# Performance work log

Measured on AMD Instinct MI355X. Metric: run time of the kernel, lower is better.

The kernel has to match this reference:

```python
import jax, jax.numpy as jnp
import numpy as np

N, D, K = 65536, 256, 4096
EPS = 1e-5
DECAY = 0.99
BN_MOMENTUM = 0.1


def setup_inputs() -> dict:
    key = jax.random.key(0)
    k1, k2, k3, k4, k5, k6 = jax.random.split(key, 6)
    return {
        "x": jax.random.normal(k1, (N, D), dtype=jnp.float32),
        "embedding": jax.random.normal(k2, (K, D), dtype=jnp.float32),
        "ema_cluster_size": jnp.zeros((K,), dtype=jnp.float32),
        "ema_w": jax.random.normal(k3, (K, D), dtype=jnp.float32),
        "running_mean": jax.random.normal(k4, (D,), dtype=jnp.float32) * 0.1,
        "running_var": jax.random.uniform(k5, (D,), dtype=jnp.float32, minval=0.5, maxval=1.5),
    }


def reference(x, embedding, ema_cluster_size, ema_w, running_mean, running_var):
    n_batch = x.shape[0]
    num_embeddings = embedding.shape[0]

    # BatchNorm1d (training mode, affine=False): normalize with batch stats
    mean = jnp.mean(x, axis=0)                       # [D]
    var = jnp.mean((x - mean) ** 2, axis=0)          # biased var, [D]
    xn = (x - mean) / jnp.sqrt(var + EPS)            # [N, D]
    # running stat updates (torch uses unbiased var for running_var)
    new_running_mean = (1.0 - BN_MOMENTUM) * running_mean + BN_MOMENTUM * mean
    var_unbiased = var * (n_batch / (n_batch - 1.0))
    new_running_var = (1.0 - BN_MOMENTUM) * running_var + BN_MOMENTUM * var_unbiased

    # squared euclidean distances [N, K]
    distances = (jnp.sum(xn ** 2, axis=1, keepdims=True)
                 + jnp.sum(embedding ** 2, axis=1)
                 - 2.0 * xn @ embedding.T)
    idx = jnp.argmin(distances, axis=1)              # [N]

    # one-hot scatter stats via segment_sum (== encodings.T contractions)
    counts = jax.ops.segment_sum(jnp.ones((n_batch,), dtype=x.dtype), idx,
                                 num_segments=num_embeddings)   # [K]
    dw = jax.ops.segment_sum(xn, idx, num_segments=num_embeddings)  # [K, D]

    # EMA updates
    new_cs = ema_cluster_size * DECAY + (1.0 - DECAY) * counts
    n_total = jnp.sum(new_cs)
    new_cs = (new_cs + 1e-5) / (n_total + num_embeddings * 1e-5) * n_total
    new_ema_w = ema_w * DECAY + (1.0 - DECAY) * dw
    new_embedding = new_ema_w / new_cs[:, None]

    running_std = jnp.sqrt(new_running_var + EPS)
    embedding_output = new_embedding * running_std[None, :] + new_running_mean[None, :]

    return (idx[:, None], new_embedding, embedding_output, new_cs, new_ema_w,
            new_running_mean, new_running_var)
```

## Files before the change

kernel.cpp:

```cpp
#include <hip/hip_runtime.h>
#include <cfloat>
#include <cmath>

#define NROWS 65536
#define DDIM 256
#define KDIM 4096

typedef short bf16x8 __attribute__((ext_vector_type(8)));
typedef float f32x4 __attribute__((ext_vector_type(4)));

constexpr float EPSV = 1e-5f;
constexpr float DECAYV = 0.99f;
constexpr float MOMV = 0.1f;
constexpr float DELTA = 1.0f;
constexpr int CAP = 16;
constexpr int SEG = 128;

constexpr size_t WS_CNT     = 0;
constexpr size_t WS_NFLAG   = WS_CNT + NROWS;
constexpr size_t WS_HIST    = WS_NFLAG + 64;
constexpr size_t WS_ZEND    = WS_HIST + KDIM;
constexpr size_t WS_START   = WS_ZEND;
constexpr size_t WS_FILLPOS = WS_START + KDIM;
constexpr size_t WS_SEGSTART= WS_FILLPOS + KDIM;
constexpr size_t WS_NSEG    = WS_SEGSTART + KDIM + 64;
constexpr size_t WS_SEGLIST = WS_NSEG + 64;
constexpr size_t WS_PARTSUM = WS_SEGLIST + 4672;
constexpr size_t WS_PARTSQ  = WS_PARTSUM + 2048 * DDIM;
constexpr size_t WS_MIDSUM  = WS_PARTSQ + 2048 * DDIM;
constexpr size_t WS_MIDSQ   = WS_MIDSUM + 256 * DDIM;
constexpr size_t WS_MEAN    = WS_MIDSQ + 256 * DDIM;
constexpr size_t WS_RSTD    = WS_MEAN + DDIM;
constexpr size_t WS_NRMEAN  = WS_RSTD + DDIM;
constexpr size_t WS_NRVAR   = WS_NRMEAN + DDIM;
constexpr size_t WS_BVEC    = WS_NRVAR + DDIM;
constexpr size_t WS_NCSRAW  = WS_BVEC + KDIM;
constexpr size_t WS_NTOT    = WS_NCSRAW + KDIM;
constexpr size_t WS_ROWINFO = WS_NTOT + 64;
constexpr size_t WS_IDX     = WS_ROWINFO + 8 * (size_t)NROWS;
constexpr size_t WS_ROWTHR  = WS_IDX + NROWS;
constexpr size_t WS_FLAG    = WS_ROWTHR + NROWS;
constexpr size_t WS_ROWLIST = WS_FLAG + NROWS;
constexpr size_t WS_CAND    = WS_ROWLIST + NROWS;
constexpr size_t WS_DWPART  = WS_CAND;
constexpr size_t WS_EPROW   = WS_CAND + (size_t)NROWS * CAP;
constexpr size_t WS_EIMG    = WS_EPROW + (size_t)KDIM * DDIM;
constexpr size_t WS_XIMG    = WS_EIMG + 524288;

constexpr size_t O_IDX   = 0;
constexpr size_t O_EMB   = NROWS;
constexpr size_t O_EOUT  = O_EMB + (size_t)KDIM * DDIM;
constexpr size_t O_CS    = O_EOUT + (size_t)KDIM * DDIM;
constexpr size_t O_EMAW  = O_CS + KDIM;
constexpr size_t O_RMEAN = O_EMAW + (size_t)KDIM * DDIM;
constexpr size_t O_RVAR  = O_RMEAN + DDIM;

__device__ inline unsigned bfpack(float a, float b) {
    unsigned ua = __float_as_uint(a), ub = __float_as_uint(b);
    ua = (ua + 0x7FFFu + ((ua >> 16) & 1u)) >> 16;
    ub = (ub + 0x7FFFu + ((ub >> 16) & 1u)) & 0xFFFF0000u;
    return (ua & 0xFFFFu) | ub;
}

__device__ inline float unpackval(float p) {
    return __uint_as_float(__float_as_uint(p) & 0xFFFFF000u);
}

#define GLOAD_LDS16(g, l) __builtin_amdgcn_global_load_lds(                       \
        (const __attribute__((address_space(1))) void*)(g),                        \
        (__attribute__((address_space(3))) void*)(l), 16, 0, 0)

__global__ __launch_bounds__(128) void k_bnpack(const float* __restrict__ x,
                                                float* __restrict__ ws) {
    const int t = threadIdx.x;
    const int b = blockIdx.x;
    char* ximg = (char*)(ws + WS_XIMG);
    float s0 = 0.f, s1 = 0.f, q0 = 0.f, q1 = 0.f;
    const int r0 = b * 32;
#pragma unroll 4
    for (int i = 0; i < 32; ++i) {
        const int r = r0 + i;
        const float2 v = *(const float2*)(x + (size_t)r * DDIM + 2 * t);
        s0 += v.x; s1 += v.y; q0 += v.x * v.x; q1 += v.y * v.y;
        const int db = (4 * t + ((r & 15) << 5)) & 511;
        *(unsigned*)(ximg + (size_t)r * 512 + db) = bfpack(v.x, v.y);
    }
    *(float2*)(ws + WS_PARTSUM + (size_t)b * DDIM + 2 * t) = make_float2(s0, s1);
    *(float2*)(ws + WS_PARTSQ  + (size_t)b * DDIM + 2 * t) = make_float2(q0, q1);
}

__global__ __launch_bounds__(256) void k_bn_mid(float* __restrict__ ws) {
    const int d = threadIdx.x, j = blockIdx.x;
    float s = 0.f, q = 0.f;
#pragma unroll
    for (int i = 0; i < 8; ++i) {
        s += ws[WS_PARTSUM + (size_t)(j * 8 + i) * DDIM + d];
        q += ws[WS_PARTSQ  + (size_t)(j * 8 + i) * DDIM + d];
    }
    ws[WS_MIDSUM + (size_t)j * DDIM + d] = s;
    ws[WS_MIDSQ  + (size_t)j * DDIM + d] = q;
}

__global__ __launch_bounds__(256) void k_bn_final(const float* __restrict__ rmean_in,
                                                  const float* __restrict__ rvar_in,
                                                  float* __restrict__ ws,
                                                  float* __restrict__ out) {
    const int d = threadIdx.x;
    float s = 0.f, sq = 0.f;
    for (int b = 0; b < 256; ++b) {
        s  += ws[WS_MIDSUM + (size_t)b * DDIM + d];
        sq += ws[WS_MIDSQ  + (size_t)b * DDIM + d];
    }
    const float mean = s / (float)NROWS;
    float var = sq / (float)NROWS - mean * mean;
    var = fmaxf(var, 0.f);
    const float rstd = 1.0f / sqrtf(var + EPSV);
    const float nrm  = (1.0f - MOMV) * rmean_in[d] + MOMV * mean;
    const float varu = var * ((float)NROWS / (float)(NROWS - 1));
    const float nrv  = (1.0f - MOMV) * rvar_in[d] + MOMV * varu;
    ws[WS_MEAN + d] = mean;
    ws[WS_RSTD + d] = rstd;
    ws[WS_NRMEAN + d] = nrm;
    ws[WS_NRVAR + d] = nrv;
    out[O_RMEAN + d] = nrm;
    out[O_RVAR + d] = nrv;
}

__global__ __launch_bounds__(128) void k_eprime(const float* __restrict__ emb,
                                                float* __restrict__ ws) {
    __shared__ float red[128];
    const int k = blockIdx.x, t = threadIdx.x;
    const int d0 = 2 * t, d1 = 2 * t + 1;
    const float em0 = emb[(size_t)k * DDIM + d0], em1 = emb[(size_t)k * DDIM + d1];
    const float rs0 = ws[WS_RSTD + d0], rs1 = ws[WS_RSTD + d1];
    const float mn0 = ws[WS_MEAN + d0], mn1 = ws[WS_MEAN + d1];
    const float e0 = em0 * rs0, e1 = em1 * rs1;
    ws[WS_EPROW + (size_t)k * DDIM + d0] = e0;
    ws[WS_EPROW + (size_t)k * DDIM + d1] = e1;
    char* img = (char*)(ws + WS_EIMG);
    const int db = (4 * t + ((k & 15) << 5)) & 511;
    *(unsigned*)(img + (size_t)k * 512 + db) = bfpack(e0, e1);
    red[t] = em0 * em0 + 2.f * mn0 * e0 + em1 * em1 + 2.f * mn1 * e1;
    __syncthreads();
    for (int s = 64; s > 0; s >>= 1) { if (t < s) red[t] += red[t + s]; __syncthreads(); }
    if (t == 0) ws[WS_BVEC + k] = red[0];
}

__global__ __launch_bounds__(256, 4) void k_gemm_min(float* __restrict__ ws) {
    extern __shared__ char smem[];
    const int t = threadIdx.x, lane = t & 63, w = t >> 6;
    const int l4 = lane & 15, kg = lane >> 4;
    const int tile = blockIdx.x >> 2;
    const int cq   = blockIdx.x & 3;
    const int rowbase = tile * 128 + w * 32;
    const char* ximg = (const char*)(ws + WS_XIMG);
    const char* eimg = (const char*)(ws + WS_EIMG) + (size_t)cq * 524288;
    const float* bvec = ws + WS_BVEC;

    bf16x8 a[2][8];
#pragma unroll
    for (int m = 0; m < 2; ++m) {
        const char* rp = ximg + (size_t)(rowbase + m * 16 + l4) * 512;
#pragma unroll
        for (int ts = 0; ts < 8; ++ts) {
            const int byte = ((kg * 16 + ts * 64) + (l4 << 5)) & 511;
            a[m][ts] = *(const bf16x8*)(rp + byte);
        }
    }

    float b1f[2][4], b2f[2][4];
#pragma unroll
    for (int m = 0; m < 2; ++m)
#pragma unroll
        for (int r = 0; r < 4; ++r) { b1f[m][r] = FLT_MAX; b2f[m][r] = FLT_MAX; }

#pragma unroll
    for (int rr = 0; rr < 4; ++rr) {
        const int off = rr * 4096 + w * 1024;
        GLOAD_LDS16(eimg + off + lane * 16, smem + off);
    }
    __syncthreads();

    for (int ch = 0; ch < 32; ++ch) {
        const char* cur = smem + (ch & 1) * 16384;
        if (ch + 1 < 32) {
            const char* src = eimg + (size_t)(ch + 1) * 16384;
            char* nb = smem + ((ch + 1) & 1) * 16384;
#pragma unroll
            for (int rr = 0; rr < 4; ++rr) {
                const int off = rr * 4096 + w * 1024;
                GLOAD_LDS16(src + off + lane * 16, nb + off);
            }
        }

        f32x4 acc[2][2];
#pragma unroll
        for (int m = 0; m < 2; ++m)
#pragma unroll
            for (int n = 0; n < 2; ++n) acc[m][n] = 0.f;

#pragma unroll
        for (int ts = 0; ts < 8; ++ts) {
            const int rot = ((kg * 16 + ts * 64) + (l4 << 5)) & 511;
            bf16x8 bfr[2];
#pragma unroll
            for (int n = 0; n < 2; ++n)
                bfr[n] = *(const bf16x8*)(cur + (n * 16 + l4) * 512 + rot);
#pragma unroll
            for (int m = 0; m < 2; ++m)
#pragma unroll
                for (int n = 0; n < 2; ++n)
                    acc[m][n] = __builtin_amdgcn_mfma_f32_16x16x32_bf16(a[m][ts], bfr[n], acc[m][n], 0, 0, 0);
        }

#pragma unroll
        for (int n = 0; n < 2; ++n) {
            const unsigned col = (unsigned)(cq * 1024 + ch * 32 + n * 16 + l4);
            const float bc = bvec[col];
#pragma unroll
            for (int m = 0; m < 2; ++m)
#pragma unroll
                for (int r = 0; r < 4; ++r) {
                    const float s = fmaf(-2.f, acc[m][n][r], bc);
                    const float p = __uint_as_float(
                        (__float_as_uint(s) & 0xFFFFF000u) | col);
                    b2f[m][r] = __builtin_amdgcn_fmed3f(p, b1f[m][r], b2f[m][r]);
                    b1f[m][r] = fminf(p, b1f[m][r]);
                }
        }
        __syncthreads();
    }

    float2* rowinfo = (float2*)(ws + WS_ROWINFO);
#pragma unroll
    for (int m = 0; m < 2; ++m)
#pragma unroll
        for (int r = 0; r < 4; ++r) {
            float v1 = b1f[m][r], v2 = b2f[m][r];
#pragma unroll
            for (int st = 1; st < 16; st <<= 1) {
                const float o1 = __shfl_xor(v1, st);
                const float o2 = __shfl_xor(v2, st);
                const float mm = fminf(v2, o2);
                v2 = __builtin_amdgcn_fmed3f(v1, o1, mm);
                v1 = fminf(v1, o1);
            }
            if (l4 == 0) {
                const int row = rowbase + m * 16 + kg * 4 + r;
                rowinfo[(size_t)row * 4 + cq] = make_float2(v1, v2);
            }
        }
}

__global__ __launch_bounds__(256) void k_flag(float* __restrict__ ws,
                                              float* __restrict__ out) {
    const int r = blockIdx.x * 256 + threadIdx.x;
    const float2* rowinfo = (const float2*)(ws + WS_ROWINFO);
    float2 q = rowinfo[(size_t)r * 4];
    float v1 = q.x, v2 = q.y;
#pragma unroll
    for (int c = 1; c < 4; ++c) {
        q = rowinfo[(size_t)r * 4 + c];
        const float mm = fminf(v2, q.y);
        v2 = __builtin_amdgcn_fmed3f(v1, q.x, mm);
        v1 = fminf(v1, q.x);
    }
    const float v1v = unpackval(v1);
    const int   i1  = (int)(__float_as_uint(v1) & 0xFFFu);
    ws[WS_ROWTHR + r] = v1v + DELTA;
    if (unpackval(v2) - v1v <= DELTA) {
        const int pos = atomicAdd((int*)(ws + WS_NFLAG), 1);
        ((int*)(ws + WS_FLAG))[pos] = r;
    } else {
        out[O_IDX + r] = (float)i1;
        ((int*)(ws + WS_IDX))[r] = i1;
        atomicAdd((int*)(ws + WS_HIST) + i1, 1);
    }
}

__global__ __launch_bounds__(256) void k_cand(float* __restrict__ ws) {
    extern __shared__ char smem[];
    const int t = threadIdx.x, lane = t & 63, w = t >> 6;
    const int l4 = lane & 15, kg = lane >> 4;
    const char* ximg = (const char*)(ws + WS_XIMG);
    const char* eimg0 = (const char*)(ws + WS_EIMG);
    const float* bvec = ws + WS_BVEC;
    const int* flag = (const int*)(ws + WS_FLAG);
    int* cnt = (int*)(ws + WS_CNT);
    int* cand = (int*)(ws + WS_CAND);
    const int nflag = *(const int*)(ws + WS_NFLAG);
    if (nflag == 0) return;
    const int ntiles = (nflag + 127) >> 7;
    const int nitems = ntiles * 8;

    for (int item = blockIdx.x; item < nitems; item += gridDim.x) {
        const int tile = item >> 3, slice = item & 7;
        const int base = tile * 128 + w * 32;
        const char* eimg = eimg0 + (size_t)slice * 262144;
        bf16x8 a[2][8];
        int frow[2][4];
        float thr[2][4];
#pragma unroll
        for (int m = 0; m < 2; ++m) {
            const int ia = base + m * 16 + l4;
            const int rowa = flag[ia < nflag ? ia : (nflag - 1)];
            const char* rp = ximg + (size_t)rowa * 512;
#pragma unroll
            for (int ts = 0; ts < 8; ++ts) {
                const int byte = ((kg * 16 + ts * 64) + ((rowa & 15) << 5)) & 511;
                a[m][ts] = *(const bf16x8*)(rp + byte);
            }
#pragma unroll
            for (int r = 0; r < 4; ++r) {
                const int ie = base + m * 16 + kg * 4 + r;
                const bool val = ie < nflag;
                const int rowe = flag[val ? ie : (nflag - 1)];
                frow[m][r] = rowe;
                thr[m][r] = val ? ws[WS_ROWTHR + rowe] : -FLT_MAX;
            }
        }
#pragma unroll
        for (int rr = 0; rr < 4; ++rr) {
            const int off = rr * 4096 + w * 1024;
            GLOAD_LDS16(eimg + off + lane * 16, smem + off);
        }
        __syncthreads();

        for (int ch = 0; ch < 16; ++ch) {
            const char* cur = smem + (ch & 1) * 16384;
            if (ch + 1 < 16) {
                const char* src = eimg + (size_t)(ch + 1) * 16384;
                char* nb = smem + ((ch + 1) & 1) * 16384;
#pragma unroll
                for (int rr = 0; rr < 4; ++rr) {
                    const int off = rr * 4096 + w * 1024;
                    GLOAD_LDS16(src + off + lane * 16, nb + off);
                }
            }
            f32x4 acc[2][2];
#pragma unroll
            for (int m = 0; m < 2; ++m)
#pragma unroll
                for (int n = 0; n < 2; ++n) acc[m][n] = 0.f;
#pragma unroll
            for (int ts = 0; ts < 8; ++ts) {
                const int rot = ((kg * 16 + ts * 64) + (l4 << 5)) & 511;
                bf16x8 bfr[2];
#pragma unroll
                for (int n = 0; n < 2; ++n)
                    bfr[n] = *(const bf16x8*)(cur + (n * 16 + l4) * 512 + rot);
#pragma unroll
                for (int m = 0; m < 2; ++m)
#pragma unroll
                    for (int n = 0; n < 2; ++n)
                        acc[m][n] = __builtin_amdgcn_mfma_f32_16x16x32_bf16(a[m][ts], bfr[n], acc[m][n], 0, 0, 0);
            }
#pragma unroll
            for (int n = 0; n < 2; ++n) {
                const int col = slice * 512 + ch * 32 + n * 16 + l4;
                const float bc = bvec[col];
#pragma unroll
                for (int m = 0; m < 2; ++m)
#pragma unroll
                    for (int r = 0; r < 4; ++r) {
                        const float s = fmaf(-2.f, acc[m][n][r], bc);
                        if (s <= thr[m][r]) {
                            const int rr2 = frow[m][r];
                            const int pos = atomicAdd(&cnt[rr2], 1);
                            if (pos < CAP) cand[(size_t)rr2 * CAP + pos] = col;
                        }
                    }
            }
            __syncthreads();
        }
    }
}

__global__ __launch_bounds__(256) void k_resolve_f(const float* __restrict__ x,
                                                   float* __restrict__ ws,
                                                   float* __restrict__ out) {
    const int t = threadIdx.x, lane = t & 63;
    const int gw = (blockIdx.x * 256 + t) >> 6;
    const int nflag = *(const int*)(ws + WS_NFLAG);
    const int* flag = (const int*)(ws + WS_FLAG);
    const int* cnt = (const int*)(ws + WS_CNT);
    const int* cand = (const int*)(ws + WS_CAND);
    const float* eprow = ws + WS_EPROW;
    const float* bvec = ws + WS_BVEC;
    int* idx_int = (int*)(ws + WS_IDX);
    for (int i = gw; i < nflag; i += 1024) {
        const int row = flag[i];
        const float4 xr = ((const float4*)(x + (size_t)row * DDIM))[lane];
        const int n = cnt[row];
        float bestv = FLT_MAX;
        int bestk = KDIM;
        if (n >= 1 && n <= CAP) {
            for (int c = 0; c < n; ++c) {
                const int k = cand[(size_t)row * CAP + c];
                const float4 er = ((const float4*)(eprow + (size_t)k * DDIM))[lane];
                float p = xr.x * er.x + xr.y * er.y + xr.z * er.z + xr.w * er.w;
                p += __shfl_xor(p, 32); p += __shfl_xor(p, 16); p += __shfl_xor(p, 8);
                p += __shfl_xor(p, 4);  p += __shfl_xor(p, 2);  p += __shfl_xor(p, 1);
                const float s = fmaf(-2.f, p, bvec[k]);
                if (s < bestv || (s == bestv && k < bestk)) { bestv = s; bestk = k; }
            }
        } else {
            for (int k = 0; k < KDIM; ++k) {
                const float4 er = ((const float4*)(eprow + (size_t)k * DDIM))[lane];
                float p = xr.x * er.x + xr.y * er.y + xr.z * er.z + xr.w * er.w;
                p += __shfl_xor(p, 32); p += __shfl_xor(p, 16); p += __shfl_xor(p, 8);
                p += __shfl_xor(p, 4);  p += __shfl_xor(p, 2);  p += __shfl_xor(p, 1);
                const float s = fmaf(-2.f, p, bvec[k]);
                if (s < bestv || (s == bestv && k < bestk)) { bestv = s; bestk = k; }
            }
        }
        if (lane == 0) {
            out[O_IDX + row] = (float)bestk;
            idx_int[row] = bestk;
            atomicAdd((int*)(ws + WS_HIST) + bestk, 1);
        }
    }
}

__global__ __launch_bounds__(256) void k_scan(const float* __restrict__ cs_in,
                                              float* __restrict__ ws) {
    __shared__ int lsum[256], lseg[256];
    __shared__ float redf[256];
    const int t = threadIdx.x;
    const int* hist = (const int*)(ws + WS_HIST);
    int h[16];
    int s = 0, g = 0;
#pragma unroll
    for (int i = 0; i < 16; ++i) {
        h[i] = hist[t * 16 + i];
        s += h[i];
        g += (h[i] + SEG - 1) / SEG;
    }
    lsum[t] = s; lseg[t] = g;
    __syncthreads();
    int v = s, u = g;
    for (int off = 1; off < 256; off <<= 1) {
        const int av = (t >= off) ? lsum[t - off] : 0;
        const int au = (t >= off) ? lseg[t - off] : 0;
        __syncthreads();
        v += av; u += au;
        lsum[t] = v; lseg[t] = u;
        __syncthreads();
    }
    int runs = v - s, rung = u - g;
    int* start = (int*)(ws + WS_START);
    int* fillpos = (int*)(ws + WS_FILLPOS);
    int* segst = (int*)(ws + WS_SEGSTART);
    int* seglist = (int*)(ws + WS_SEGLIST);
    float emapart = 0.f;
#pragma unroll
    for (int i = 0; i < 16; ++i) {
        const int k = t * 16 + i;
        start[k] = runs;
        fillpos[k] = runs;
        segst[k] = rung;
        const int ns = (h[i] + SEG - 1) / SEG;
        for (int j = 0; j < ns; ++j) seglist[rung + j] = (k << 10) | j;
        runs += h[i];
        rung += ns;
        const float ncs = cs_in[k] * DECAYV + (1.0f - DECAYV) * (float)h[i];
        ws[WS_NCSRAW + k] = ncs;
        emapart += ncs;
    }
    if (t == 255) {
        segst[KDIM] = rung;
        *(int*)(ws + WS_NSEG) = rung;
    }
    redf[t] = emapart;
    __syncthreads();
    for (int ss = 128; ss > 0; ss >>= 1) { if (t < ss) redf[t] += redf[t + ss]; __syncthreads(); }
    if (t == 0) ws[WS_NTOT] = redf[0];
}

__global__ __launch_bounds__(256) void k_fill(float* __restrict__ ws) {
    const int r = blockIdx.x * 256 + threadIdx.x;
    const int k = ((const int*)(ws + WS_IDX))[r];
    const int pos = atomicAdd((int*)(ws + WS_FILLPOS) + k, 1);
    ((int*)(ws + WS_ROWLIST))[pos] = r;
}

__global__ __launch_bounds__(256) void k_gather_seg(const float* __restrict__ x,
                                                    float* __restrict__ ws) {
    const int b = blockIdx.x;
    if (b >= *(const int*)(ws + WS_NSEG)) return;
    const int e = ((const int*)(ws + WS_SEGLIST))[b];
    const int k = e >> 10, j = e & 1023;
    const int base = ((const int*)(ws + WS_START))[k];
    const int n = ((const int*)(ws + WS_HIST))[k];
    const int st = base + j * SEG;
    const int en = min(st + SEG, base + n);
    const int* rowlist = (const int*)(ws + WS_ROWLIST);
    const int d = threadIdx.x;
    float s0 = 0.f, s1 = 0.f, s2 = 0.f, s3 = 0.f;
    int i = st;
    for (; i + 3 < en; i += 4) {
        s0 += x[(size_t)rowlist[i]     * DDIM + d];
        s1 += x[(size_t)rowlist[i + 1] * DDIM + d];
        s2 += x[(size_t)rowlist[i + 2] * DDIM + d];
        s3 += x[(size_t)rowlist[i + 3] * DDIM + d];
    }
    for (; i < en; ++i) s0 += x[(size_t)rowlist[i] * DDIM + d];
    (ws + WS_DWPART)[(size_t)b * DDIM + d] = (s0 + s1) + (s2 + s3);
}

__global__ __launch_bounds__(256) void k_final(const float* __restrict__ ema_w,
                                               const float* __restrict__ ws,
                                               float* __restrict__ out) {
    const int k = blockIdx.x;
    const int d = threadIdx.x;
    const int* segst = (const int*)(ws + WS_SEGSTART);
    const int ss = segst[k];
    const int ns = segst[k + 1] - ss;
    const float* dwpart = ws + WS_DWPART;
    float a0 = 0.f, a1 = 0.f;
    int j = 0;
    for (; j + 1 < ns; j += 2) {
        a0 += dwpart[(size_t)(ss + j)     * DDIM + d];
        a1 += dwpart[(size_t)(ss + j + 1) * DDIM + d];
    }
    if (j < ns) a0 += dwpart[(size_t)(ss + j) * DDIM + d];
    const float dwsum = a0 + a1;
    const int n = ((const int*)(ws + WS_HIST))[k];
    const float ntot = ws[WS_NTOT];
    const float ncs  = (ws[WS_NCSRAW + k] + 1e-5f) / (ntot + (float)KDIM * 1e-5f) * ntot;
    const float mn   = ws[WS_MEAN + d];
    const float rs   = ws[WS_RSTD + d];
    const size_t e   = (size_t)k * DDIM + d;
    const float dw   = (dwsum - (float)n * mn) * rs;
    const float nw   = ema_w[e] * DECAYV + (1.0f - DECAYV) * dw;
    const float nemb = nw / ncs;
    const float eo   = nemb * sqrtf(ws[WS_NRVAR + d] + EPSV) + ws[WS_NRMEAN + d];
    out[O_EMB + e]  = nemb;
    out[O_EOUT + e] = eo;
    out[O_EMAW + e] = nw;
    if (d == 0) out[O_CS + k] = ncs;
}

extern "C" void kernel_launch(void* const* d_in, const int* in_sizes, int n_in,
                              void* d_out, int out_size, void* d_ws, size_t ws_size,
                              hipStream_t stream) {
    const float* x     = (const float*)d_in[0];
    const float* emb   = (const float*)d_in[1];
    const float* cs    = (const float*)d_in[2];
    const float* ema_w = (const float*)d_in[3];
    const float* rmean = (const float*)d_in[4];
    const float* rvar  = (const float*)d_in[5];
    float* out = (float*)d_out;
    float* ws  = (float*)d_ws;

    hipMemsetAsync(ws, 0, WS_ZEND * sizeof(float), stream);

    k_bnpack<<<2048, 128, 0, stream>>>(x, ws);
    k_bn_mid<<<256, 256, 0, stream>>>(ws);
    k_bn_final<<<1, 256, 0, stream>>>(rmean, rvar, ws, out);
    k_eprime<<<KDIM, 128, 0, stream>>>(emb, ws);

    constexpr int LDSB = 32768;
    k_gemm_min<<<2048, 256, LDSB, stream>>>(ws);
    k_flag<<<NROWS / 256, 256, 0, stream>>>(ws, out);
    k_cand<<<512, 256, LDSB, stream>>>(ws);
    k_resolve_f<<<256, 256, 0, stream>>>(x, ws, out);

    k_scan<<<1, 256, 0, stream>>>(cs, ws);
    k_fill<<<NROWS / 256, 256, 0, stream>>>(ws);
    k_gather_seg<<<4608, 256, 0, stream>>>(x, ws);
    k_final<<<KDIM, 256, 0, stream>>>(ema_w, ws, out);
}
```

Baseline: 325.4 us.

## Vectorize auxiliary kernels with float4 accesses and tune GEMM occupancy and unroll

Rewrites k_bnpack, k_eprime, k_gather_seg and k_final so each thread uses float4 loads and stores. k_eprime replaces its shared-memory tree reduction with wavefront shuffles and packs four codebook rows per block. k_gather_seg splits the rows across four wavefronts and combines their partial sums through shared memory. k_gemm_min gets a higher launch-bounds occupancy hint and an unroll-2 pragma on its chunk loop. The aim is fewer memory transactions and launches in the bandwidth-bound side kernels, at the risk of register spills in the GEMM from the tighter occupancy target.

```diff
diff --git a/kernel.cpp b/kernel.cpp
--- a/kernel.cpp
+++ b/kernel.cpp
@@ -70,23 +70,27 @@
         (const __attribute__((address_space(1))) void*)(g),                        \
         (__attribute__((address_space(3))) void*)(l), 16, 0, 0)
 
-__global__ __launch_bounds__(128) void k_bnpack(const float* __restrict__ x,
+__global__ __launch_bounds__(256) void k_bnpack(const float* __restrict__ x,
                                                 float* __restrict__ ws) {
     const int t = threadIdx.x;
-    const int b = blockIdx.x;
+    const int q = t & 63, g = t >> 6;
+    const int r0 = blockIdx.x * 128 + g * 32;
     char* ximg = (char*)(ws + WS_XIMG);
-    float s0 = 0.f, s1 = 0.f, q0 = 0.f, q1 = 0.f;
-    const int r0 = b * 32;
+    const float4* x4 = (const float4*)x;
+    float4 s = make_float4(0.f, 0.f, 0.f, 0.f);
+    float4 sq = make_float4(0.f, 0.f, 0.f, 0.f);
 #pragma unroll 4
     for (int i = 0; i < 32; ++i) {
         const int r = r0 + i;
-        const float2 v = *(const float2*)(x + (size_t)r * DDIM + 2 * t);
-        s0 += v.x; s1 += v.y; q0 += v.x * v.x; q1 += v.y * v.y;
-        const int db = (4 * t + ((r & 15) << 5)) & 511;
-        *(unsigned*)(ximg + (size_t)r * 512 + db) = bfpack(v.x, v.y);
-    }
-    *(float2*)(ws + WS_PARTSUM + (size_t)b * DDIM + 2 * t) = make_float2(s0, s1);
-    *(float2*)(ws + WS_PARTSQ  + (size_t)b * DDIM + 2 * t) = make_float2(q0, q1);
+        const float4 v = x4[(size_t)r * 64 + q];
+        s.x += v.x; s.y += v.y; s.z += v.z; s.w += v.w;
+        sq.x += v.x * v.x; sq.y += v.y * v.y; sq.z += v.z * v.z; sq.w += v.w * v.w;
+        const int db = (8 * q + ((r & 15) << 5)) & 511;
+        *(uint2*)(ximg + (size_t)r * 512 + db) = make_uint2(bfpack(v.x, v.y), bfpack(v.z, v.w));
+    }
+    const size_t p = (size_t)(blockIdx.x * 4 + g) * 64 + q;
+    ((float4*)(ws + WS_PARTSUM))[p] = s;
+    ((float4*)(ws + WS_PARTSQ))[p]  = sq;
 }
 
 __global__ __launch_bounds__(256) void k_bn_mid(float* __restrict__ ws) {
@@ -126,27 +130,27 @@
     out[O_RVAR + d] = nrv;
 }
 
-__global__ __launch_bounds__(128) void k_eprime(const float* __restrict__ emb,
+__global__ __launch_bounds__(256) void k_eprime(const float* __restrict__ emb,
                                                 float* __restrict__ ws) {
-    __shared__ float red[128];
-    const int k = blockIdx.x, t = threadIdx.x;
-    const int d0 = 2 * t, d1 = 2 * t + 1;
-    const float em0 = emb[(size_t)k * DDIM + d0], em1 = emb[(size_t)k * DDIM + d1];
-    const float rs0 = ws[WS_RSTD + d0], rs1 = ws[WS_RSTD + d1];
-    const float mn0 = ws[WS_MEAN + d0], mn1 = ws[WS_MEAN + d1];
-    const float e0 = em0 * rs0, e1 = em1 * rs1;
-    ws[WS_EPROW + (size_t)k * DDIM + d0] = e0;
-    ws[WS_EPROW + (size_t)k * DDIM + d1] = e1;
+    const int t = threadIdx.x, l = t & 63, w = t >> 6;
+    const int k = blockIdx.x * 4 + w;
+    const float4 em = ((const float4*)emb)[(size_t)k * 64 + l];
+    const float4 rs = ((const float4*)(ws + WS_RSTD))[l];
+    const float4 mn = ((const float4*)(ws + WS_MEAN))[l];
+    float4 e;
+    e.x = em.x * rs.x; e.y = em.y * rs.y; e.z = em.z * rs.z; e.w = em.w * rs.w;
+    ((float4*)(ws + WS_EPROW))[(size_t)k * 64 + l] = e;
     char* img = (char*)(ws + WS_EIMG);
-    const int db = (4 * t + ((k & 15) << 5)) & 511;
-    *(unsigned*)(img + (size_t)k * 512 + db) = bfpack(e0, e1);
-    red[t] = em0 * em0 + 2.f * mn0 * e0 + em1 * em1 + 2.f * mn1 * e1;
-    __syncthreads();
-    for (int s = 64; s > 0; s >>= 1) { if (t < s) red[t] += red[t + s]; __syncthreads(); }
-    if (t == 0) ws[WS_BVEC + k] = red[0];
-}
-
-__global__ __launch_bounds__(256, 4) void k_gemm_min(float* __restrict__ ws) {
+    const int db = (8 * l + ((k & 15) << 5)) & 511;
+    *(uint2*)(img + (size_t)k * 512 + db) = make_uint2(bfpack(e.x, e.y), bfpack(e.z, e.w));
+    float red = em.x * em.x + 2.f * mn.x * e.x + em.y * em.y + 2.f * mn.y * e.y
+              + em.z * em.z + 2.f * mn.z * e.z + em.w * em.w + 2.f * mn.w * e.w;
+    red += __shfl_xor(red, 32); red += __shfl_xor(red, 16); red += __shfl_xor(red, 8);
+    red += __shfl_xor(red, 4);  red += __shfl_xor(red, 2);  red += __shfl_xor(red, 1);
+    if (l == 0) ws[WS_BVEC + k] = red;
+}
+
+__global__ __launch_bounds__(256, 5) void k_gemm_min(float* __restrict__ ws) {
     extern __shared__ char smem[];
     const int t = threadIdx.x, lane = t & 63, w = t >> 6;
     const int l4 = lane & 15, kg = lane >> 4;
@@ -181,6 +185,7 @@
     }
     __syncthreads();
 
+#pragma unroll 2
     for (int ch = 0; ch < 32; ++ch) {
         const char* cur = smem + (ch & 1) * 16384;
         if (ch + 1 < 32) {
@@ -486,6 +491,7 @@
 
 __global__ __launch_bounds__(256) void k_gather_seg(const float* __restrict__ x,
                                                     float* __restrict__ ws) {
+    __shared__ float4 ls[4][64];
     const int b = blockIdx.x;
     if (b >= *(const int*)(ws + WS_NSEG)) return;
     const int e = ((const int*)(ws + WS_SEGLIST))[b];
@@ -495,50 +501,65 @@
     const int st = base + j * SEG;
     const int en = min(st + SEG, base + n);
     const int* rowlist = (const int*)(ws + WS_ROWLIST);
-    const int d = threadIdx.x;
-    float s0 = 0.f, s1 = 0.f, s2 = 0.f, s3 = 0.f;
-    int i = st;
-    for (; i + 3 < en; i += 4) {
-        s0 += x[(size_t)rowlist[i]     * DDIM + d];
-        s1 += x[(size_t)rowlist[i + 1] * DDIM + d];
-        s2 += x[(size_t)rowlist[i + 2] * DDIM + d];
-        s3 += x[(size_t)rowlist[i + 3] * DDIM + d];
-    }
-    for (; i < en; ++i) s0 += x[(size_t)rowlist[i] * DDIM + d];
-    (ws + WS_DWPART)[(size_t)b * DDIM + d] = (s0 + s1) + (s2 + s3);
-}
-
-__global__ __launch_bounds__(256) void k_final(const float* __restrict__ ema_w,
-                                               const float* __restrict__ ws,
-                                               float* __restrict__ out) {
+    const int t = threadIdx.x, q = t & 63, g = t >> 6;
+    const float4* x4 = (const float4*)x;
+    float4 s = make_float4(0.f, 0.f, 0.f, 0.f);
+    for (int i = st + g; i < en; i += 4) {
+        const float4 v = x4[(size_t)rowlist[i] * 64 + q];
+        s.x += v.x; s.y += v.y; s.z += v.z; s.w += v.w;
+    }
+    ls[g][q] = s;
+    __syncthreads();
+    if (t < 64) {
+        const float4 a0 = ls[0][t], a1 = ls[1][t], a2 = ls[2][t], a3 = ls[3][t];
+        float4 r;
+        r.x = (a0.x + a1.x) + (a2.x + a3.x);
+        r.y = (a0.y + a1.y) + (a2.y + a3.y);
+        r.z = (a0.z + a1.z) + (a2.z + a3.z);
+        r.w = (a0.w + a1.w) + (a2.w + a3.w);
+        ((float4*)(ws + WS_DWPART))[(size_t)b * 64 + t] = r;
+    }
+}
+
+__global__ __launch_bounds__(64) void k_final(const float* __restrict__ ema_w,
+                                              const float* __restrict__ ws,
+                                              float* __restrict__ out) {
     const int k = blockIdx.x;
-    const int d = threadIdx.x;
+    const int q = threadIdx.x;
     const int* segst = (const int*)(ws + WS_SEGSTART);
     const int ss = segst[k];
     const int ns = segst[k + 1] - ss;
-    const float* dwpart = ws + WS_DWPART;
-    float a0 = 0.f, a1 = 0.f;
-    int j = 0;
-    for (; j + 1 < ns; j += 2) {
-        a0 += dwpart[(size_t)(ss + j)     * DDIM + d];
-        a1 += dwpart[(size_t)(ss + j + 1) * DDIM + d];
-    }
-    if (j < ns) a0 += dwpart[(size_t)(ss + j) * DDIM + d];
-    const float dwsum = a0 + a1;
+    const float4* dwpart = (const float4*)(ws + WS_DWPART);
+    float4 a = make_float4(0.f, 0.f, 0.f, 0.f);
+    for (int j = 0; j < ns; ++j) {
+        const float4 v = dwpart[(size_t)(ss + j) * 64 + q];
+        a.x += v.x; a.y += v.y; a.z += v.z; a.w += v.w;
+    }
     const int n = ((const int*)(ws + WS_HIST))[k];
     const float ntot = ws[WS_NTOT];
     const float ncs  = (ws[WS_NCSRAW + k] + 1e-5f) / (ntot + (float)KDIM * 1e-5f) * ntot;
-    const float mn   = ws[WS_MEAN + d];
-    const float rs   = ws[WS_RSTD + d];
-    const size_t e   = (size_t)k * DDIM + d;
-    const float dw   = (dwsum - (float)n * mn) * rs;
-    const float nw   = ema_w[e] * DECAYV + (1.0f - DECAYV) * dw;
-    const float nemb = nw / ncs;
-    const float eo   = nemb * sqrtf(ws[WS_NRVAR + d] + EPSV) + ws[WS_NRMEAN + d];
-    out[O_EMB + e]  = nemb;
-    out[O_EOUT + e] = eo;
-    out[O_EMAW + e] = nw;
-    if (d == 0) out[O_CS + k] = ncs;
+    const float4 mn = ((const float4*)(ws + WS_MEAN))[q];
+    const float4 rs = ((const float4*)(ws + WS_RSTD))[q];
+    const float4 nrv = ((const float4*)(ws + WS_NRVAR))[q];
+    const float4 nrm = ((const float4*)(ws + WS_NRMEAN))[q];
+    const float4 ew = ((const float4*)ema_w)[(size_t)k * 64 + q];
+    const float fn = (float)n;
+    float4 nwv, nembv, eov;
+    nwv.x = ew.x * DECAYV + (1.f - DECAYV) * ((a.x - fn * mn.x) * rs.x);
+    nwv.y = ew.y * DECAYV + (1.f - DECAYV) * ((a.y - fn * mn.y) * rs.y);
+    nwv.z = ew.z * DECAYV + (1.f - DECAYV) * ((a.z - fn * mn.z) * rs.z);
+    nwv.w = ew.w * DECAYV + (1.f - DECAYV) * ((a.w - fn * mn.w) * rs.w);
+    const float inv = 1.0f / ncs;
+    nembv.x = nwv.x * inv; nembv.y = nwv.y * inv;
+    nembv.z = nwv.z * inv; nembv.w = nwv.w * inv;
+    eov.x = nembv.x * sqrtf(nrv.x + EPSV) + nrm.x;
+    eov.y = nembv.y * sqrtf(nrv.y + EPSV) + nrm.y;
+    eov.z = nembv.z * sqrtf(nrv.z + EPSV) + nrm.z;
+    eov.w = nembv.w * sqrtf(nrv.w + EPSV) + nrm.w;
+    ((float4*)(out + O_EMB))[(size_t)k * 64 + q]  = nembv;
+    ((float4*)(out + O_EOUT))[(size_t)k * 64 + q] = eov;
+    ((float4*)(out + O_EMAW))[(size_t)k * 64 + q] = nwv;
+    if (q == 0) out[O_CS + k] = ncs;
 }
 
 extern "C" void kernel_launch(void* const* d_in, const int* in_sizes, int n_in,
@@ -555,10 +576,10 @@
 
     hipMemsetAsync(ws, 0, WS_ZEND * sizeof(float), stream);
 
-    k_bnpack<<<2048, 128, 0, stream>>>(x, ws);
+    k_bnpack<<<512, 256, 0, stream>>>(x, ws);
     k_bn_mid<<<256, 256, 0, stream>>>(ws);
     k_bn_final<<<1, 256, 0, stream>>>(rmean, rvar, ws, out);
-    k_eprime<<<KDIM, 128, 0, stream>>>(emb, ws);
+    k_eprime<<<KDIM / 4, 256, 0, stream>>>(emb, ws);
 
     constexpr int LDSB = 32768;
     k_gemm_min<<<2048, 256, LDSB, stream>>>(ws);
@@ -569,5 +590,5 @@
     k_scan<<<1, 256, 0, stream>>>(cs, ws);
     k_fill<<<NROWS / 256, 256, 0, stream>>>(ws);
     k_gather_seg<<<4608, 256, 0, stream>>>(x, ws);
-    k_final<<<KDIM, 256, 0, stream>>>(ema_w, ws, out);
-}
+    k_final<<<KDIM, 64, 0, stream>>>(ema_w, ws, out);
+}
```

New measurement: 673.3 us. 107% more time.
